# Optimization experiments

Hardware: AMD Instinct MI355X
Metric: run time of the kernel (lower is better)

The kernel has to match this reference:

```python
import jax, jax.numpy as jnp
import numpy as np

N = 500000
IN_C = 128
OUT_C = 128


def setup_inputs() -> dict:
    key = jax.random.key(0)
    k1, k2, k3, k4 = jax.random.split(key, 4)
    x = jax.random.normal(k1, (N, IN_C), dtype=jnp.float32)
    # E must equal N for the original `out + out[col]` broadcast to be valid
    edge_index = jax.random.randint(k2, (2, N), 0, N, dtype=jnp.int64)
    # Linear(in_channels, out_channels): W [out, in], b [out]
    bound = 1.0 / np.sqrt(IN_C)
    W = jax.random.uniform(k3, (OUT_C, IN_C), dtype=jnp.float32, minval=-bound, maxval=bound)
    b = jax.random.uniform(k4, (OUT_C,), dtype=jnp.float32, minval=-bound, maxval=bound)
    return {"x": x, "edge_index": edge_index, "W": W, "b": b}


def reference(x, edge_index, W, b):
    row, col = edge_index[0], edge_index[1]
    out = x @ W.T + b                      # [N, C] dense projection
    # gather rows by col, then scatter-add +1 at positions row (duplicates accumulate)
    agg = out[col].at[row].add(jnp.float32(1.0))  # [E, C], E == N
    return out + agg
```

## Files before the change

kernel.cpp:

```cpp
#include <hip/hip_runtime.h>
#include <hip/hip_bf16.h>
#include <stdint.h>

typedef __attribute__((ext_vector_type(8))) __bf16 bf16x8;
typedef __attribute__((ext_vector_type(4))) float floatx4;

#define C 128
#define BROWS 128

__device__ __forceinline__ __bf16 f2b(float f) {
  return __builtin_bit_cast(__bf16, __float2bfloat16(f));
}

__global__ void prep_kernel(const int* __restrict__ rowidx, const float* __restrict__ W,
                            int* __restrict__ deg, __bf16* __restrict__ Wb, int n) {
  int i = blockIdx.x * blockDim.x + threadIdx.x;
  if (i < C * C) Wb[i] = f2b(W[i]);
  if (i < n) atomicAdd(deg + rowidx[i], 1);
}

__launch_bounds__(512, 6)
__global__ void gconv_kernel(const float* __restrict__ x,
                             const int* __restrict__ colidx,
                             const __bf16* __restrict__ Wb,
                             const float* __restrict__ bias,
                             const int* __restrict__ deg,
                             float* __restrict__ out, int n) {
  __shared__ bf16x8 sW[2048];

  const int t = threadIdx.x;
  const int lane = t & 63, w = t >> 6;
  const int l15 = lane & 15, quad = lane >> 4;

  const int base = blockIdx.x * BROWS + w * 16;

  int ga  = base + l15;
  int gal = ga < n ? ga : n - 1;
  int cg  = colidx[gal];

  {
    int r = t >> 2, q = t & 3, rx = r & 15;
    const bf16x8* src = (const bf16x8*)(Wb + r * C) + q * 4;
    bf16x8 wreg[4];
#pragma unroll
    for (int i = 0; i < 4; i++) wreg[i] = src[i];
#pragma unroll
    for (int i = 0; i < 4; i++) sW[r * 16 + ((q * 4 + i) ^ rx)] = wreg[i];
  }

  const floatx4* pa = (const floatx4*)(x + (size_t)gal * C) + quad * 2;
  const floatx4* pc = (const floatx4*)(x + (size_t)cg  * C) + quad * 2;
  floatx4 va[8], vc[8];
#pragma unroll
  for (int kc = 0; kc < 4; kc++) {
    va[2 * kc]     = pa[kc * 8];
    va[2 * kc + 1] = pa[kc * 8 + 1];
    vc[2 * kc]     = pc[kc * 8];
    vc[2 * kc + 1] = pc[kc * 8 + 1];
  }

  int gr  = base + quad * 4;
  int grl = (gr + 3 < n) ? gr : ((n - 4) & ~3);
  int4 d4 = *(const int4*)(deg + grl);

  float b2[8];
#pragma unroll
  for (int tt = 0; tt < 8; tt++) b2[tt] = 2.0f * bias[tt * 16 + l15];

  __syncthreads();

  bf16x8 av[4];
#pragma unroll
  for (int kc = 0; kc < 4; kc++) {
    floatx4 a0 = va[2 * kc], a1 = va[2 * kc + 1];
    floatx4 c0 = vc[2 * kc], c1 = vc[2 * kc + 1];
    av[kc][0] = f2b(a0[0] + c0[0]); av[kc][1] = f2b(a0[1] + c0[1]);
    av[kc][2] = f2b(a0[2] + c0[2]); av[kc][3] = f2b(a0[3] + c0[3]);
    av[kc][4] = f2b(a1[0] + c1[0]); av[kc][5] = f2b(a1[1] + c1[1]);
    av[kc][6] = f2b(a1[2] + c1[2]); av[kc][7] = f2b(a1[3] + c1[3]);
  }

  const bf16x8* wr0 = sW + l15 * 16 + ((quad + 0)  ^ l15);
  const bf16x8* wr1 = sW + l15 * 16 + ((quad + 4)  ^ l15);
  const bf16x8* wr2 = sW + l15 * 16 + ((quad + 8)  ^ l15);
  const bf16x8* wr3 = sW + l15 * 16 + ((quad + 12) ^ l15);

  floatx4 acc[8];
#pragma unroll
  for (int i = 0; i < 8; i++) acc[i] = (floatx4){0.f, 0.f, 0.f, 0.f};

#pragma unroll
  for (int tt = 0; tt < 8; tt++) {
    acc[tt] = __builtin_amdgcn_mfma_f32_16x16x32_bf16(av[0], wr0[tt * 256], acc[tt], 0, 0, 0);
    acc[tt] = __builtin_amdgcn_mfma_f32_16x16x32_bf16(av[1], wr1[tt * 256], acc[tt], 0, 0, 0);
    acc[tt] = __builtin_amdgcn_mfma_f32_16x16x32_bf16(av[2], wr2[tt * 256], acc[tt], 0, 0, 0);
    acc[tt] = __builtin_amdgcn_mfma_f32_16x16x32_bf16(av[3], wr3[tt * 256], acc[tt], 0, 0, 0);
  }

  float dvf[4];
  dvf[0] = (float)d4.x; dvf[1] = (float)d4.y;
  dvf[2] = (float)d4.z; dvf[3] = (float)d4.w;
#pragma unroll
  for (int r = 0; r < 4; r++) {
    int g = gr + r;
    if (g < n) {
      float* orow = out + (size_t)g * C + l15;
      float dv = dvf[r];
#pragma unroll
      for (int tt = 0; tt < 8; tt++) orow[tt * 16] = acc[tt][r] + b2[tt] + dv;
    }
  }
}

extern "C" void kernel_launch(void* const* d_in, const int* in_sizes, int n_in,
                              void* d_out, int out_size, void* d_ws, size_t ws_size,
                              hipStream_t stream) {
  const float* x    = (const float*)d_in[0];
  const int*   edge = (const int*)d_in[1];
  const float* W    = (const float*)d_in[2];
  const float* bias = (const float*)d_in[3];
  float* out = (float*)d_out;

  const int n = in_sizes[0] / C;

  int* deg = (int*)d_ws;
  size_t wb_off = ((size_t)n * sizeof(int) + 255) & ~(size_t)255;
  __bf16* Wb = (__bf16*)((char*)d_ws + wb_off);

  hipMemsetAsync(deg, 0, (size_t)n * sizeof(int), stream);

  int nb = (n + 255) / 256;
  prep_kernel<<<nb, 256, 0, stream>>>(edge, W, deg, Wb, n);

  int mb = (n + BROWS - 1) / BROWS;
  gconv_kernel<<<mb, 512, 0, stream>>>(x, edge + n, Wb, bias, deg, out, n);
}
```

Baseline: 520.4 us.

## Stage x rows and gathered rows into LDS via direct global-to-LDS loads

Result: faster. 494.2 us (-5.0%).

```diff
diff --git a/kernel.cpp b/kernel.cpp
--- a/kernel.cpp
+++ b/kernel.cpp
@@ -6,10 +6,16 @@
 typedef __attribute__((ext_vector_type(4))) float floatx4;
 
 #define C 128
-#define BROWS 128
+#define BROWS 64
 
 __device__ __forceinline__ __bf16 f2b(float f) {
   return __builtin_bit_cast(__bf16, __float2bfloat16(f));
+}
+
+__device__ __forceinline__ void gl2lds16(const void* g, void* l) {
+  __builtin_amdgcn_global_load_lds(
+      (const __attribute__((address_space(1))) void*)g,
+      (__attribute__((address_space(3))) void*)l, 16, 0, 0);
 }
 
 __global__ void prep_kernel(const int* __restrict__ rowidx, const float* __restrict__ W,
@@ -19,7 +25,7 @@
   if (i < n) atomicAdd(deg + rowidx[i], 1);
 }
 
-__launch_bounds__(512, 6)
+__launch_bounds__(256, 1)
 __global__ void gconv_kernel(const float* __restrict__ x,
                              const int* __restrict__ colidx,
                              const __bf16* __restrict__ Wb,
@@ -27,39 +33,42 @@
                              const int* __restrict__ deg,
                              float* __restrict__ out, int n) {
   __shared__ bf16x8 sW[2048];
+  __shared__ float sD[BROWS * 128];
+  __shared__ float sG[BROWS * 128];
 
   const int t = threadIdx.x;
   const int lane = t & 63, w = t >> 6;
   const int l15 = lane & 15, quad = lane >> 4;
+  const int l31 = lane & 31, half = lane >> 5;
+  const int base = blockIdx.x * BROWS;
 
-  const int base = blockIdx.x * BROWS + w * 16;
+  int gidx = base + w * 16 + l15;
+  int cv = colidx[gidx < n ? gidx : n - 1];
 
-  int ga  = base + l15;
-  int gal = ga < n ? ga : n - 1;
-  int cg  = colidx[gal];
-
-  {
-    int r = t >> 2, q = t & 3, rx = r & 15;
-    const bf16x8* src = (const bf16x8*)(Wb + r * C) + q * 4;
-    bf16x8 wreg[4];
 #pragma unroll
-    for (int i = 0; i < 4; i++) wreg[i] = src[i];
-#pragma unroll
-    for (int i = 0; i < 4; i++) sW[r * 16 + ((q * 4 + i) ^ rx)] = wreg[i];
+  for (int i = 0; i < 8; i++) {
+    int r = w * 32 + i * 4 + (lane >> 4);
+    const __bf16* src = Wb + r * C + (((lane & 15) ^ (r & 15)) << 3);
+    gl2lds16(src, &sW[(w * 32 + i * 4) * 16]);
   }
 
-  const floatx4* pa = (const floatx4*)(x + (size_t)gal * C) + quad * 2;
-  const floatx4* pc = (const floatx4*)(x + (size_t)cg  * C) + quad * 2;
-  floatx4 va[8], vc[8];
 #pragma unroll
-  for (int kc = 0; kc < 4; kc++) {
-    va[2 * kc]     = pa[kc * 8];
-    va[2 * kc + 1] = pa[kc * 8 + 1];
-    vc[2 * kc]     = pc[kc * 8];
-    vc[2 * kc + 1] = pc[kc * 8 + 1];
+  for (int i = 0; i < 8; i++) {
+    int rl = w * 16 + i * 2 + half;
+    int gi = base + rl; if (gi >= n) gi = n - 1;
+    const float* src = x + (size_t)gi * C + ((l31 ^ (rl & 7)) << 2);
+    gl2lds16(src, &sD[(w * 16 + i * 2) * 128]);
   }
 
-  int gr  = base + quad * 4;
+#pragma unroll
+  for (int i = 0; i < 8; i++) {
+    int rl = w * 16 + i * 2 + half;
+    int cg = __shfl(cv, i * 2 + half);
+    const float* src = x + (size_t)cg * C + ((l31 ^ (rl & 7)) << 2);
+    gl2lds16(src, &sG[(w * 16 + i * 2) * 128]);
+  }
+
+  int gr  = base + w * 16 + quad * 4;
   int grl = (gr + 3 < n) ? gr : ((n - 4) & ~3);
   int4 d4 = *(const int4*)(deg + grl);
 
@@ -69,15 +78,22 @@
 
   __syncthreads();
 
+  const float* dR = sD + (w * 16 + l15) * 128;
+  const float* gR = sG + (w * 16 + l15) * 128;
+  const int s7 = l15 & 7;
+
   bf16x8 av[4];
 #pragma unroll
   for (int kc = 0; kc < 4; kc++) {
-    floatx4 a0 = va[2 * kc], a1 = va[2 * kc + 1];
-    floatx4 c0 = vc[2 * kc], c1 = vc[2 * kc + 1];
-    av[kc][0] = f2b(a0[0] + c0[0]); av[kc][1] = f2b(a0[1] + c0[1]);
-    av[kc][2] = f2b(a0[2] + c0[2]); av[kc][3] = f2b(a0[3] + c0[3]);
-    av[kc][4] = f2b(a1[0] + c1[0]); av[kc][5] = f2b(a1[1] + c1[1]);
-    av[kc][6] = f2b(a1[2] + c1[2]); av[kc][7] = f2b(a1[3] + c1[3]);
+    int c0 = 2 * quad + 8 * kc;
+    floatx4 d0 = *(const floatx4*)(dR + (((c0)     ^ s7) << 2));
+    floatx4 d1 = *(const floatx4*)(dR + (((c0 + 1) ^ s7) << 2));
+    floatx4 g0 = *(const floatx4*)(gR + (((c0)     ^ s7) << 2));
+    floatx4 g1 = *(const floatx4*)(gR + (((c0 + 1) ^ s7) << 2));
+    av[kc][0] = f2b(d0[0] + g0[0]); av[kc][1] = f2b(d0[1] + g0[1]);
+    av[kc][2] = f2b(d0[2] + g0[2]); av[kc][3] = f2b(d0[3] + g0[3]);
+    av[kc][4] = f2b(d1[0] + g1[0]); av[kc][5] = f2b(d1[1] + g1[1]);
+    av[kc][6] = f2b(d1[2] + g1[2]); av[kc][7] = f2b(d1[3] + g1[3]);
   }
 
   const bf16x8* wr0 = sW + l15 * 16 + ((quad + 0)  ^ l15);
@@ -133,5 +149,5 @@
   prep_kernel<<<nb, 256, 0, stream>>>(edge, W, deg, Wb, n);
 
   int mb = (n + BROWS - 1) / BROWS;
-  gconv_kernel<<<mb, 512, 0, stream>>>(x, edge + n, Wb, bias, deg, out, n);
+  gconv_kernel<<<mb, 256, 0, stream>>>(x, edge + n, Wb, bias, deg, out, n);
 }
```
